# Kernel tuning notes

Measured on AMD Instinct MI355X. Metric: run time of the kernel, lower is better.

## Reference

```python
import jax, jax.numpy as jnp
import numpy as np

N_NODES = 50000
N_EDGES = 800000
N_FEAT = 128
N_CLASSES = 64
K_HOPS = 2


def setup_inputs() -> dict:
    key = jax.random.key(0)
    k1, k2, k3, k4 = jax.random.split(key, 4)
    x = jax.random.normal(k1, (N_NODES, N_FEAT), dtype=jnp.float32)
    edge_index = jax.random.randint(k2, (2, N_EDGES), 0, N_NODES, dtype=jnp.int64)
    # Linear(num_features -> num_classes) params (PyG SGConv lin layer)
    lim = 1.0 / np.sqrt(N_FEAT)
    W = jax.random.uniform(k3, (N_CLASSES, N_FEAT), minval=-lim, maxval=lim, dtype=jnp.float32)
    b = jax.random.uniform(k4, (N_CLASSES,), minval=-lim, maxval=lim, dtype=jnp.float32)
    return {"x": x, "edge_index": edge_index, "W": W, "b": b}


def reference(x, edge_index, W, b):
    N = x.shape[0]
    # gcn_norm: add self-loops, symmetric normalization deg^-1/2 A_hat deg^-1/2
    loop = jnp.arange(N, dtype=edge_index.dtype)
    src = jnp.concatenate([edge_index[0], loop])  # message sources j
    dst = jnp.concatenate([edge_index[1], loop])  # message targets i
    deg = jax.ops.segment_sum(jnp.ones_like(src, dtype=x.dtype), dst, num_segments=N)
    dinv = jnp.where(deg > 0, jax.lax.rsqrt(deg), 0.0)
    norm = dinv[src] * dinv[dst]  # [E+N]
    # K=2 hops of SpMM: out[i] = sum_{j->i} norm * x[j]
    for _ in range(K_HOPS):
        x = jax.ops.segment_sum(norm[:, None] * x[src], dst, num_segments=N)
    logits = x @ W.T + b  # [N, num_classes]
    return jax.nn.log_softmax(logits, axis=1)
```

## Files before the change

kernel.cpp:

```cpp
#include <hip/hip_runtime.h>
#include <hip/hip_fp16.h>
#include <math.h>

#define NFEAT 128
#define NCLS  64
#define RQ    16
#define WSTR  132
#define NBLK  256


typedef _Float16 h2v __attribute__((ext_vector_type(2)));

__device__ __forceinline__ float dot2acc(unsigned int hv, unsigned int wv, float c) {
#if __has_builtin(__builtin_amdgcn_fdot2)
    union { unsigned int u; h2v v; } a, bq; a.u = hv; bq.u = wv;
    return __builtin_amdgcn_fdot2(a.v, bq.v, c, false);
#else
    union { unsigned int u; __half2 h; } a, bq; a.u = hv; bq.u = wv;
    float2 fa = __half22float2(a.h), fb = __half22float2(bq.h);
    return fmaf(fa.x, fb.x, fmaf(fa.y, fb.y, c));
#endif
}

__device__ __forceinline__ void acc4(__half2 a[4], uint4 v) {
    union { uint4 u; __half2 h[4]; } c; c.u = v;
    a[0] = __hadd2(a[0], c.h[0]); a[1] = __hadd2(a[1], c.h[1]);
    a[2] = __hadd2(a[2], c.h[2]); a[3] = __hadd2(a[3], c.h[3]);
}

__device__ __forceinline__ __half2 red2(__half2 a) {
    union { __half2 h; int i; } u, v;
    u.h = a; v.i = __shfl_xor(u.i, 16); a = __hadd2(a, v.h);
    u.h = a; v.i = __shfl_xor(u.i, 32); a = __hadd2(a, v.h);
    return a;
}

__global__ __launch_bounds__(256) void hist_kernel(const int* __restrict__ dst,
                                                   int* __restrict__ h,
                                                   int E4, int E, int nb) {
    __shared__ int lh[256];
    const int tid = threadIdx.x;
    lh[tid] = 0;
    __syncthreads();
    for (int idx = blockIdx.x * 256 + tid; idx < E4; idx += NBLK * 256) {
        int base = idx * 4;
        if (base + 3 < E) {
            int4 d = ((const int4*)dst)[idx];
            atomicAdd(&lh[d.x >> 8], 1); atomicAdd(&lh[d.y >> 8], 1);
            atomicAdd(&lh[d.z >> 8], 1); atomicAdd(&lh[d.w >> 8], 1);
        } else {
            for (int e = base; e < E; ++e) atomicAdd(&lh[dst[e] >> 8], 1);
        }
    }
    __syncthreads();
    if (tid < nb) h[blockIdx.x * nb + tid] = lh[tid];
}

__global__ __launch_bounds__(256) void colscan_kernel(int* __restrict__ h,
                                                      int* __restrict__ btot, int nb) {
    __shared__ int lds[256];
    const int tid = threadIdx.x;
    const int B = blockIdx.x;
    int v = h[tid * nb + B];
    lds[tid] = v;
    __syncthreads();
    for (int off = 1; off < 256; off <<= 1) {
        int t = (tid >= off) ? lds[tid - off] : 0;
        __syncthreads();
        lds[tid] += t;
        __syncthreads();
    }
    h[tid * nb + B] = lds[tid] - v;
    if (tid == 255) btot[B] = lds[255];
}

__global__ __launch_bounds__(256) void bucket_scan_kernel(const int* __restrict__ btot,
                                                          int* __restrict__ bbase, int nb) {
    __shared__ int lds[256];
    const int tid = threadIdx.x;
    int v = (tid < nb) ? btot[tid] : 0;
    lds[tid] = v;
    __syncthreads();
    for (int off = 1; off < 256; off <<= 1) {
        int t = (tid >= off) ? lds[tid - off] : 0;
        __syncthreads();
        lds[tid] += t;
        __syncthreads();
    }
    if (tid < nb) bbase[tid + 1] = lds[tid];
    if (tid == 0) bbase[0] = 0;
}

__global__ __launch_bounds__(256) void bucket_scatter_kernel(const int* __restrict__ src,
                                                             const int* __restrict__ dst,
                                                             const int* __restrict__ h,
                                                             const int* __restrict__ bbase,
                                                             int2* __restrict__ bedg,
                                                             int E4, int E, int nb) {
    __shared__ int cur[256];
    const int tid = threadIdx.x;
    if (tid < nb) cur[tid] = bbase[tid] + h[blockIdx.x * nb + tid];
    __syncthreads();
    for (int idx = blockIdx.x * 256 + tid; idx < E4; idx += NBLK * 256) {
        int base = idx * 4;
        if (base + 3 < E) {
            int4 s = ((const int4*)src)[idx];
            int4 d = ((const int4*)dst)[idx];
            int p;
            p = atomicAdd(&cur[d.x >> 8], 1); bedg[p] = make_int2(s.x, d.x);
            p = atomicAdd(&cur[d.y >> 8], 1); bedg[p] = make_int2(s.y, d.y);
            p = atomicAdd(&cur[d.z >> 8], 1); bedg[p] = make_int2(s.z, d.z);
            p = atomicAdd(&cur[d.w >> 8], 1); bedg[p] = make_int2(s.w, d.w);
        } else {
            for (int e = base; e < E; ++e) {
                int p = atomicAdd(&cur[dst[e] >> 8], 1);
                bedg[p] = make_int2(src[e], dst[e]);
            }
        }
    }
}

__global__ __launch_bounds__(256) void drain_kernel(const int2* __restrict__ bedg,
                                                    const int* __restrict__ bbase,
                                                    int* __restrict__ csr,
                                                    int* __restrict__ rbeg,
                                                    int* __restrict__ rend,
                                                    float* __restrict__ dinv, int N) {
    __shared__ int lcnt[256];
    __shared__ int lds[256];
    __shared__ int loc[256];
    const int B = blockIdx.x;
    const int tid = threadIdx.x;
    const int s0 = bbase[B], s1 = bbase[B + 1];

    lcnt[tid] = 0;
    __syncthreads();
    for (int e = s0 + tid; e < s1; e += 256)
        atomicAdd(&lcnt[bedg[e].y & 255], 1);
    __syncthreads();

    const int c = lcnt[tid];
    const int cp = (c + 3) & ~3;
    lds[tid] = cp;
    __syncthreads();
    for (int off = 1; off < 256; off <<= 1) {
        int t = (tid >= off) ? lds[tid - off] : 0;
        __syncthreads();
        lds[tid] += t;
        __syncthreads();
    }
    const int base = bbase[B] + 768 * B;
    loc[tid] = base + lds[tid] - cp;
    __syncthreads();
    lcnt[tid] = loc[tid];
    __syncthreads();

    for (int e = s0 + tid; e < s1; e += 256) {
        int2 Ev = bedg[e];
        int p = atomicAdd(&lcnt[Ev.y & 255], 1);
        csr[p] = Ev.x;
    }
    __syncthreads();

    int i = B * 256 + tid;
    if (i < N) {
        int start = loc[tid], end = start + cp;
        for (int p = lcnt[tid]; p < end; ++p) csr[p] = N;
        rbeg[i] = start; rend[i] = end;
        dinv[i] = rsqrtf((float)c + 1.0f);
    }
}

__global__ void prep_kernel(const float* __restrict__ x, const float* __restrict__ dinv,
                            __half* __restrict__ xh, __half* __restrict__ y1h, int N) {
    int idx = blockIdx.x * blockDim.x + threadIdx.x;
    int total = N * 32;
    if (idx < total) {
        float d = dinv[idx >> 5];
        float4 v = ((const float4*)x)[idx];
        union { uint2 u; __half2 h[2]; } r;
        r.h[0] = __floats2half2_rn(d * v.x, d * v.y);
        r.h[1] = __floats2half2_rn(d * v.z, d * v.w);
        ((uint2*)xh)[idx] = r.u;
    } else if (idx < total + 32) {
        ((uint2*)xh)[idx] = uint2{0, 0};
    } else if (idx < total + 64) {
        ((uint2*)y1h)[idx - 32] = uint2{0, 0};
    }
}

__device__ __forceinline__ void gather_row(__half2 a[4], const uint4* __restrict__ X,
                                           const int* __restrict__ csr,
                                           int ks, int ke, int sub, int q, int Nd) {
    int k = ks;
    int j0, j1, j2, j3;
    bool have = (k + 16 <= ke);
    if (have) {
        j0 = csr[k + sub]; j1 = csr[k + 4 + sub];
        j2 = csr[k + 8 + sub]; j3 = csr[k + 12 + sub];
    }
    while (have) {
        uint4 v0 = X[(size_t)j0 * RQ + q];
        uint4 v1 = X[(size_t)j1 * RQ + q];
        uint4 v2 = X[(size_t)j2 * RQ + q];
        uint4 v3 = X[(size_t)j3 * RQ + q];
        k += 16;
        have = (k + 16 <= ke);
        if (have) {
            j0 = csr[k + sub]; j1 = csr[k + 4 + sub];
            j2 = csr[k + 8 + sub]; j3 = csr[k + 12 + sub];
        }
        acc4(a, v0); acc4(a, v1); acc4(a, v2); acc4(a, v3);
    }
    int rem = (ke - k) >> 2;
    if (rem) {
        int t0 = csr[k + sub];
        int t1 = csr[k + 4 + sub];
        int t2 = csr[k + 8 + sub];
        if (rem < 2) t1 = Nd;
        if (rem < 3) t2 = Nd;
        uint4 v0 = X[(size_t)t0 * RQ + q];
        uint4 v1 = X[(size_t)t1 * RQ + q];
        uint4 v2 = X[(size_t)t2 * RQ + q];
        acc4(a, v0); acc4(a, v1); acc4(a, v2);
    }
}

template <int SQUARE>
__global__ __launch_bounds__(256) void hop_kernel(const __half* __restrict__ in_h,
                                                  const float* __restrict__ dinv,
                                                  const int* __restrict__ rbeg,
                                                  const int* __restrict__ rend,
                                                  const int* __restrict__ csr,
                                                  __half* __restrict__ out_h, int N) {
    const int tid = threadIdx.x;
    const int w = tid >> 6, lane = tid & 63;
    const int i = blockIdx.x * 4 + w;
    if (i >= N) return;
    const int sub = lane >> 4;
    const int q = lane & 15;
    const uint4* X = (const uint4*)in_h;

    __half2 a[4];
    a[0] = __float2half2_rn(0.f); a[1] = a[0]; a[2] = a[0]; a[3] = a[0];

    int ks = rbeg[i], ke = rend[i];
    gather_row(a, X, csr, ks, ke, sub, q, N);
    if (sub == 0) acc4(a, X[(size_t)i * RQ + q]);

    a[0] = red2(a[0]); a[1] = red2(a[1]); a[2] = red2(a[2]); a[3] = red2(a[3]);

    if (sub == 0) {
        float di = dinv[i];
        float s = SQUARE ? di * di : di;
        union { uint4 u; __half2 h[4]; } r;
        #pragma unroll
        for (int t = 0; t < 4; ++t) {
            float2 f = __half22float2(a[t]);
            r.h[t] = __floats2half2_rn(s * f.x, s * f.y);
        }
        ((uint4*)out_h)[(size_t)i * RQ + q] = r.u;
    }
}

__global__ __launch_bounds__(512) void cls_kernel(const __half* __restrict__ x2h,
                                                  const float* __restrict__ W,
                                                  const float* __restrict__ b,
                                                  float* __restrict__ out, int N) {
    __shared__ __half Wl[NCLS * WSTR];
    __shared__ __align__(16) __half HT[64][NFEAT];

    const int tid = threadIdx.x;
    const int w = tid >> 6, lane = tid & 63;

    for (int e = tid; e < NCLS * NFEAT; e += 512) {
        int r = e >> 7, c = e & 127;
        Wl[r * WSTR + c] = __float2half(W[e]);
    }
    const size_t base = (size_t)blockIdx.x * 64 * NFEAT;
    {
        const uint4* src = (const uint4*)(x2h + base);
        uint4* dst = (uint4*)&HT[0][0];
        dst[tid] = src[tid];
        dst[tid + 512] = src[tid + 512];
    }
    __syncthreads();

    unsigned int wreg[64];
    {
        const uint2* wr = (const uint2*)&Wl[lane * WSTR];
        #pragma unroll
        for (int t = 0; t < 32; ++t) {
            uint2 v = wr[t];
            wreg[2 * t] = v.x; wreg[2 * t + 1] = v.y;
        }
    }
    const float breg = b[lane];

    #pragma unroll 1
    for (int r = 0; r < 8; ++r) {
        int node = blockIdx.x * 64 + w * 8 + r;
        if (node >= N) break;
        const unsigned int* hrow = (const unsigned int*)&HT[w * 8 + r][0];
        float dot = breg;
        #pragma unroll
        for (int t = 0; t < 64; ++t)
            dot = dot2acc(hrow[t], wreg[t], dot);

        float m = dot;
        for (int o = 32; o > 0; o >>= 1) m = fmaxf(m, __shfl_xor(m, o));
        float ex = __expf(dot - m);
        float se = ex;
        for (int o = 32; o > 0; o >>= 1) se += __shfl_xor(se, o);
        out[(size_t)node * NCLS + lane] = dot - m - logf(se);
    }
}


static inline size_t align256(size_t v) { return (v + 255) & ~(size_t)255; }

extern "C" void kernel_launch(void* const* d_in, const int* in_sizes, int n_in,
                              void* d_out, int out_size, void* d_ws, size_t ws_size,
                              hipStream_t stream) {
    const float* x  = (const float*)d_in[0];
    const int*   ei = (const int*)d_in[1];
    const float* W  = (const float*)d_in[2];
    const float* b  = (const float*)d_in[3];
    float* out = (float*)d_out;

    const int N = in_sizes[0] / NFEAT;
    const int E = in_sizes[1] / 2;
    const int* src = ei;
    const int* dst = ei + E;
    const int NBUCK = (N + 255) >> 8;

    const int CSR_CAP = E + 768 * NBUCK + 64;

    char* ws = (char*)d_ws;
    size_t o = 0;
    int*    h     = (int*)(ws + o);    o += align256((size_t)NBLK * NBUCK * 4);
    int*    btot  = (int*)(ws + o);    o += align256(256 * 4);
    int*    bbase = (int*)(ws + o);    o += align256(257 * 4);
    int2*   bedg  = (int2*)(ws + o);   o += align256((size_t)E * 8);
    int*    csr   = (int*)(ws + o);    o += align256((size_t)CSR_CAP * 4);
    int*    rbeg  = (int*)(ws + o);    o += align256((size_t)N * 4);
    int*    rend  = (int*)(ws + o);    o += align256((size_t)N * 4);
    float*  dinv  = (float*)(ws + o);  o += align256((size_t)N * 4);
    __half* xh    = (__half*)(ws + o); o += align256((size_t)(N + 64) * NFEAT * 2);
    __half* y1h   = (__half*)(ws + o); o += align256((size_t)(N + 1) * NFEAT * 2);
    __half* x2h   = xh;

    const int E4 = (E + 3) / 4;

    hist_kernel<<<NBLK, 256, 0, stream>>>(dst, h, E4, E, NBUCK);
    colscan_kernel<<<NBUCK, 256, 0, stream>>>(h, btot, NBUCK);
    bucket_scan_kernel<<<1, 256, 0, stream>>>(btot, bbase, NBUCK);
    bucket_scatter_kernel<<<NBLK, 256, 0, stream>>>(src, dst, h, bbase, bedg, E4, E, NBUCK);
    drain_kernel<<<NBUCK, 256, 0, stream>>>(bedg, bbase, csr, rbeg, rend, dinv, N);
    prep_kernel<<<(N * 32 + 64 + 255) / 256, 256, 0, stream>>>(x, dinv, xh, y1h, N);
    hop_kernel<1><<<(N + 3) / 4, 256, 0, stream>>>(xh, dinv, rbeg, rend, csr, y1h, N);
    hop_kernel<0><<<(N + 3) / 4, 256, 0, stream>>>(y1h, dinv, rbeg, rend, csr, x2h, N);
    cls_kernel<<<(N + 63) / 64, 512, 0, stream>>>(x2h, W, b, out, N);
}
```

Measured before the change: 190.1 us.

## Apply linear layer before propagation to gather 64-wide rows and fuse softmax

Uses linearity to apply W to x first, so both SpMM hops gather 64-feature half rows instead of 128-feature rows, halving gather bandwidth. The prep kernel is folded into the GEMM, and the second hop is fused with bias add and log-softmax. CSR rows are padded to multiples of 8 to match the new 8-way lane split, which adds padding entries. Half-precision accumulation now runs over projected values, which changes rounding behaviour.

Result: faster. 161.4 us (-15.1%).

```diff
diff --git a/kernel.cpp b/kernel.cpp
--- a/kernel.cpp
+++ b/kernel.cpp
@@ -4,7 +4,7 @@
 
 #define NFEAT 128
 #define NCLS  64
-#define RQ    16
+#define RQ8   8
 #define WSTR  132
 #define NBLK  256
 
@@ -28,8 +28,9 @@
     a[2] = __hadd2(a[2], c.h[2]); a[3] = __hadd2(a[3], c.h[3]);
 }
 
-__device__ __forceinline__ __half2 red2(__half2 a) {
+__device__ __forceinline__ __half2 red8(__half2 a) {
     union { __half2 h; int i; } u, v;
+    u.h = a; v.i = __shfl_xor(u.i, 8);  a = __hadd2(a, v.h);
     u.h = a; v.i = __shfl_xor(u.i, 16); a = __hadd2(a, v.h);
     u.h = a; v.i = __shfl_xor(u.i, 32); a = __hadd2(a, v.h);
     return a;
@@ -140,7 +141,7 @@
     __syncthreads();
 
     const int c = lcnt[tid];
-    const int cp = (c + 3) & ~3;
+    const int cp = (c + 7) & ~7;
     lds[tid] = cp;
     __syncthreads();
     for (int off = 1; off < 256; off <<= 1) {
@@ -149,7 +150,7 @@
         lds[tid] += t;
         __syncthreads();
     }
-    const int base = bbase[B] + 768 * B;
+    const int base = bbase[B] + 1792 * B;
     loc[tid] = base + lds[tid] - cp;
     __syncthreads();
     lcnt[tid] = loc[tid];
@@ -171,118 +172,39 @@
     }
 }
 
-__global__ void prep_kernel(const float* __restrict__ x, const float* __restrict__ dinv,
-                            __half* __restrict__ xh, __half* __restrict__ y1h, int N) {
-    int idx = blockIdx.x * blockDim.x + threadIdx.x;
-    int total = N * 32;
-    if (idx < total) {
-        float d = dinv[idx >> 5];
-        float4 v = ((const float4*)x)[idx];
-        union { uint2 u; __half2 h[2]; } r;
-        r.h[0] = __floats2half2_rn(d * v.x, d * v.y);
-        r.h[1] = __floats2half2_rn(d * v.z, d * v.w);
-        ((uint2*)xh)[idx] = r.u;
-    } else if (idx < total + 32) {
-        ((uint2*)xh)[idx] = uint2{0, 0};
-    } else if (idx < total + 64) {
-        ((uint2*)y1h)[idx - 32] = uint2{0, 0};
-    }
-}
-
-__device__ __forceinline__ void gather_row(__half2 a[4], const uint4* __restrict__ X,
-                                           const int* __restrict__ csr,
-                                           int ks, int ke, int sub, int q, int Nd) {
-    int k = ks;
-    int j0, j1, j2, j3;
-    bool have = (k + 16 <= ke);
-    if (have) {
-        j0 = csr[k + sub]; j1 = csr[k + 4 + sub];
-        j2 = csr[k + 8 + sub]; j3 = csr[k + 12 + sub];
-    }
-    while (have) {
-        uint4 v0 = X[(size_t)j0 * RQ + q];
-        uint4 v1 = X[(size_t)j1 * RQ + q];
-        uint4 v2 = X[(size_t)j2 * RQ + q];
-        uint4 v3 = X[(size_t)j3 * RQ + q];
-        k += 16;
-        have = (k + 16 <= ke);
-        if (have) {
-            j0 = csr[k + sub]; j1 = csr[k + 4 + sub];
-            j2 = csr[k + 8 + sub]; j3 = csr[k + 12 + sub];
-        }
-        acc4(a, v0); acc4(a, v1); acc4(a, v2); acc4(a, v3);
-    }
-    int rem = (ke - k) >> 2;
-    if (rem) {
-        int t0 = csr[k + sub];
-        int t1 = csr[k + 4 + sub];
-        int t2 = csr[k + 8 + sub];
-        if (rem < 2) t1 = Nd;
-        if (rem < 3) t2 = Nd;
-        uint4 v0 = X[(size_t)t0 * RQ + q];
-        uint4 v1 = X[(size_t)t1 * RQ + q];
-        uint4 v2 = X[(size_t)t2 * RQ + q];
-        acc4(a, v0); acc4(a, v1); acc4(a, v2);
-    }
-}
-
-template <int SQUARE>
-__global__ __launch_bounds__(256) void hop_kernel(const __half* __restrict__ in_h,
-                                                  const float* __restrict__ dinv,
-                                                  const int* __restrict__ rbeg,
-                                                  const int* __restrict__ rend,
-                                                  const int* __restrict__ csr,
-                                                  __half* __restrict__ out_h, int N) {
-    const int tid = threadIdx.x;
-    const int w = tid >> 6, lane = tid & 63;
-    const int i = blockIdx.x * 4 + w;
-    if (i >= N) return;
-    const int sub = lane >> 4;
-    const int q = lane & 15;
-    const uint4* X = (const uint4*)in_h;
-
-    __half2 a[4];
-    a[0] = __float2half2_rn(0.f); a[1] = a[0]; a[2] = a[0]; a[3] = a[0];
-
-    int ks = rbeg[i], ke = rend[i];
-    gather_row(a, X, csr, ks, ke, sub, q, N);
-    if (sub == 0) acc4(a, X[(size_t)i * RQ + q]);
-
-    a[0] = red2(a[0]); a[1] = red2(a[1]); a[2] = red2(a[2]); a[3] = red2(a[3]);
-
-    if (sub == 0) {
-        float di = dinv[i];
-        float s = SQUARE ? di * di : di;
-        union { uint4 u; __half2 h[4]; } r;
-        #pragma unroll
-        for (int t = 0; t < 4; ++t) {
-            float2 f = __half22float2(a[t]);
-            r.h[t] = __floats2half2_rn(s * f.x, s * f.y);
-        }
-        ((uint4*)out_h)[(size_t)i * RQ + q] = r.u;
-    }
-}
-
-__global__ __launch_bounds__(512) void cls_kernel(const __half* __restrict__ x2h,
-                                                  const float* __restrict__ W,
-                                                  const float* __restrict__ b,
-                                                  float* __restrict__ out, int N) {
+__global__ __launch_bounds__(512) void gemm_kernel(const float* __restrict__ x,
+                                                   const float* __restrict__ W,
+                                                   const float* __restrict__ dinv,
+                                                   __half* __restrict__ zh,
+                                                   __half* __restrict__ y1h, int N) {
     __shared__ __half Wl[NCLS * WSTR];
     __shared__ __align__(16) __half HT[64][NFEAT];
 
     const int tid = threadIdx.x;
     const int w = tid >> 6, lane = tid & 63;
+
+    if (blockIdx.x == 0 && tid < 32) {
+        if (tid < 16) ((uint2*)zh)[(size_t)N * 16 + tid] = uint2{0u, 0u};
+        else          ((uint2*)y1h)[(size_t)N * 16 + (tid - 16)] = uint2{0u, 0u};
+    }
 
     for (int e = tid; e < NCLS * NFEAT; e += 512) {
         int r = e >> 7, c = e & 127;
         Wl[r * WSTR + c] = __float2half(W[e]);
     }
-    const size_t base = (size_t)blockIdx.x * 64 * NFEAT;
     {
-        const uint4* src = (const uint4*)(x2h + base);
-        uint4* dst = (uint4*)&HT[0][0];
-        dst[tid] = src[tid];
-        dst[tid + 512] = src[tid + 512];
+        const float4* srcf = (const float4*)(x + (size_t)blockIdx.x * 64 * NFEAT);
+        uint2* dh = (uint2*)&HT[0][0];
+        const int row0 = blockIdx.x * 64;
+        #pragma unroll
+        for (int t = 0; t < 4; ++t) {
+            int e = tid + 512 * t;
+            float4 f = (row0 + (e >> 5) < N) ? srcf[e] : float4{0.f, 0.f, 0.f, 0.f};
+            union { uint2 u; __half2 h[2]; } r;
+            r.h[0] = __floats2half2_rn(f.x, f.y);
+            r.h[1] = __floats2half2_rn(f.z, f.w);
+            dh[e] = r.u;
+        }
     }
     __syncthreads();
 
@@ -295,24 +217,146 @@
             wreg[2 * t] = v.x; wreg[2 * t + 1] = v.y;
         }
     }
-    const float breg = b[lane];
 
     #pragma unroll 1
     for (int r = 0; r < 8; ++r) {
         int node = blockIdx.x * 64 + w * 8 + r;
         if (node >= N) break;
         const unsigned int* hrow = (const unsigned int*)&HT[w * 8 + r][0];
-        float dot = breg;
+        float dot = 0.f;
         #pragma unroll
         for (int t = 0; t < 64; ++t)
             dot = dot2acc(hrow[t], wreg[t], dot);
-
-        float m = dot;
-        for (int o = 32; o > 0; o >>= 1) m = fmaxf(m, __shfl_xor(m, o));
-        float ex = __expf(dot - m);
-        float se = ex;
-        for (int o = 32; o > 0; o >>= 1) se += __shfl_xor(se, o);
-        out[(size_t)node * NCLS + lane] = dot - m - logf(se);
+        zh[(size_t)node * NCLS + lane] = __float2half(dinv[node] * dot);
+    }
+}
+
+__device__ __forceinline__ void gather_row64(__half2 a[4], const uint4* __restrict__ X,
+                                             const int* __restrict__ csr,
+                                             int ks, int ke, int sub, int q, int Nd) {
+    int k = ks;
+    int j0, j1, j2, j3;
+    bool have = (k + 32 <= ke);
+    if (have) {
+        j0 = csr[k + sub];      j1 = csr[k + 8 + sub];
+        j2 = csr[k + 16 + sub]; j3 = csr[k + 24 + sub];
+    }
+    while (have) {
+        uint4 v0 = X[(size_t)j0 * RQ8 + q];
+        uint4 v1 = X[(size_t)j1 * RQ8 + q];
+        uint4 v2 = X[(size_t)j2 * RQ8 + q];
+        uint4 v3 = X[(size_t)j3 * RQ8 + q];
+        k += 32;
+        have = (k + 32 <= ke);
+        if (have) {
+            j0 = csr[k + sub];      j1 = csr[k + 8 + sub];
+            j2 = csr[k + 16 + sub]; j3 = csr[k + 24 + sub];
+        }
+        acc4(a, v0); acc4(a, v1); acc4(a, v2); acc4(a, v3);
+    }
+    int rem = (ke - k) >> 3;
+    if (rem) {
+        int t0 = csr[k + sub];
+        int t1 = csr[k + 8 + sub];
+        int t2 = csr[k + 16 + sub];
+        if (rem < 2) t1 = Nd;
+        if (rem < 3) t2 = Nd;
+        uint4 v0 = X[(size_t)t0 * RQ8 + q];
+        uint4 v1 = X[(size_t)t1 * RQ8 + q];
+        uint4 v2 = X[(size_t)t2 * RQ8 + q];
+        acc4(a, v0); acc4(a, v1); acc4(a, v2);
+    }
+}
+
+template <int SQUARE>
+__global__ __launch_bounds__(256) void hop64_kernel(const __half* __restrict__ in_h,
+                                                    const float* __restrict__ dinv,
+                                                    const int* __restrict__ rbeg,
+                                                    const int* __restrict__ rend,
+                                                    const int* __restrict__ csr,
+                                                    __half* __restrict__ out_h, int N) {
+    const int tid = threadIdx.x;
+    const int w = tid >> 6, lane = tid & 63;
+    const int i = blockIdx.x * 4 + w;
+    if (i >= N) return;
+    const int sub = lane >> 3;
+    const int q = lane & 7;
+    const uint4* X = (const uint4*)in_h;
+
+    __half2 a[4];
+    a[0] = __float2half2_rn(0.f); a[1] = a[0]; a[2] = a[0]; a[3] = a[0];
+
+    int ks = rbeg[i], ke = rend[i];
+    gather_row64(a, X, csr, ks, ke, sub, q, N);
+    if (sub == 0) acc4(a, X[(size_t)i * RQ8 + q]);
+
+    a[0] = red8(a[0]); a[1] = red8(a[1]); a[2] = red8(a[2]); a[3] = red8(a[3]);
+
+    if (sub == 0) {
+        float di = dinv[i];
+        float s = SQUARE ? di * di : di;
+        union { uint4 u; __half2 h[4]; } r;
+        #pragma unroll
+        for (int t = 0; t < 4; ++t) {
+            float2 f = __half22float2(a[t]);
+            r.h[t] = __floats2half2_rn(s * f.x, s * f.y);
+        }
+        ((uint4*)out_h)[(size_t)i * RQ8 + q] = r.u;
+    }
+}
+
+__global__ __launch_bounds__(256) void hop2cls_kernel(const __half* __restrict__ in_h,
+                                                      const float* __restrict__ dinv,
+                                                      const int* __restrict__ rbeg,
+                                                      const int* __restrict__ rend,
+                                                      const int* __restrict__ csr,
+                                                      const float* __restrict__ b,
+                                                      float* __restrict__ out, int N) {
+    const int tid = threadIdx.x;
+    const int w = tid >> 6, lane = tid & 63;
+    const int i = blockIdx.x * 4 + w;
+    if (i >= N) return;
+    const int sub = lane >> 3;
+    const int q = lane & 7;
+    const uint4* X = (const uint4*)in_h;
+
+    float4 b0 = ((const float4*)b)[q * 2];
+    float4 b1 = ((const float4*)b)[q * 2 + 1];
+
+    __half2 a[4];
+    a[0] = __float2half2_rn(0.f); a[1] = a[0]; a[2] = a[0]; a[3] = a[0];
+
+    int ks = rbeg[i], ke = rend[i];
+    gather_row64(a, X, csr, ks, ke, sub, q, N);
+    if (sub == 0) acc4(a, X[(size_t)i * RQ8 + q]);
+
+    a[0] = red8(a[0]); a[1] = red8(a[1]); a[2] = red8(a[2]); a[3] = red8(a[3]);
+
+    if (sub == 0) {
+        float di = dinv[i];
+        float f[8];
+        float2 p;
+        p = __half22float2(a[0]); f[0] = fmaf(di, p.x, b0.x); f[1] = fmaf(di, p.y, b0.y);
+        p = __half22float2(a[1]); f[2] = fmaf(di, p.x, b0.z); f[3] = fmaf(di, p.y, b0.w);
+        p = __half22float2(a[2]); f[4] = fmaf(di, p.x, b1.x); f[5] = fmaf(di, p.y, b1.y);
+        p = __half22float2(a[3]); f[6] = fmaf(di, p.x, b1.z); f[7] = fmaf(di, p.y, b1.w);
+        float m = f[0];
+        #pragma unroll
+        for (int t = 1; t < 8; ++t) m = fmaxf(m, f[t]);
+        m = fmaxf(m, __shfl_xor(m, 1));
+        m = fmaxf(m, __shfl_xor(m, 2));
+        m = fmaxf(m, __shfl_xor(m, 4));
+        float se = 0.f;
+        #pragma unroll
+        for (int t = 0; t < 8; ++t) se += __expf(f[t] - m);
+        se += __shfl_xor(se, 1);
+        se += __shfl_xor(se, 2);
+        se += __shfl_xor(se, 4);
+        float ls = m + logf(se);
+        float4 o0 = {f[0] - ls, f[1] - ls, f[2] - ls, f[3] - ls};
+        float4 o1 = {f[4] - ls, f[5] - ls, f[6] - ls, f[7] - ls};
+        float4* op = (float4*)(out + (size_t)i * NCLS);
+        op[q * 2] = o0; op[q * 2 + 1] = o1;
     }
 }
 
@@ -334,7 +378,7 @@
     const int* dst = ei + E;
     const int NBUCK = (N + 255) >> 8;
 
-    const int CSR_CAP = E + 768 * NBUCK + 64;
+    const int CSR_CAP = E + 1792 * NBUCK + 64;
 
     char* ws = (char*)d_ws;
     size_t o = 0;
@@ -346,9 +390,8 @@
     int*    rbeg  = (int*)(ws + o);    o += align256((size_t)N * 4);
     int*    rend  = (int*)(ws + o);    o += align256((size_t)N * 4);
     float*  dinv  = (float*)(ws + o);  o += align256((size_t)N * 4);
-    __half* xh    = (__half*)(ws + o); o += align256((size_t)(N + 64) * NFEAT * 2);
-    __half* y1h   = (__half*)(ws + o); o += align256((size_t)(N + 1) * NFEAT * 2);
-    __half* x2h   = xh;
+    __half* zh    = (__half*)(ws + o); o += align256((size_t)(N + 1) * NCLS * 2);
+    __half* y1h   = (__half*)(ws + o); o += align256((size_t)(N + 1) * NCLS * 2);
 
     const int E4 = (E + 3) / 4;
 
@@ -357,8 +400,7 @@
     bucket_scan_kernel<<<1, 256, 0, stream>>>(btot, bbase, NBUCK);
     bucket_scatter_kernel<<<NBLK, 256, 0, stream>>>(src, dst, h, bbase, bedg, E4, E, NBUCK);
     drain_kernel<<<NBUCK, 256, 0, stream>>>(bedg, bbase, csr, rbeg, rend, dinv, N);
-    prep_kernel<<<(N * 32 + 64 + 255) / 256, 256, 0, stream>>>(x, dinv, xh, y1h, N);
-    hop_kernel<1><<<(N + 3) / 4, 256, 0, stream>>>(xh, dinv, rbeg, rend, csr, y1h, N);
-    hop_kernel<0><<<(N + 3) / 4, 256, 0, stream>>>(y1h, dinv, rbeg, rend, csr, x2h, N);
-    cls_kernel<<<(N + 63) / 64, 512, 0, stream>>>(x2h, W, b, out, N);
-}
+    gemm_kernel<<<(N + 63) / 64, 512, 0, stream>>>(x, W, dinv, zh, y1h, N);
+    hop64_kernel<1><<<(N + 3) / 4, 256, 0, stream>>>(zh, dinv, rbeg, rend, csr, y1h, N);
+    hop2cls_kernel<<<(N + 3) / 4, 256, 0, stream>>>(y1h, dinv, rbeg, rend, csr, b, out, N);
+}
```
